# Kernel optimization log

Measured on AMD Instinct MI355X. Metric: run time of the kernel, lower is better.

## Reference

```python
import jax, jax.numpy as jnp
import numpy as np

HIDDEN = 1024
HEADS = 16
HEAD_DIM = HIDDEN // HEADS
SCALE = HEAD_DIM ** -0.5


def setup_inputs() -> dict:
    key = jax.random.key(0)
    kx, kw, ko = jax.random.split(key, 3)
    x = jax.random.normal(kx, (2, 2048, HIDDEN), dtype=jnp.float32)
    # nn.Linear(hidden, 3*hidden, bias=False): weight shape [3*hidden, hidden]
    w_qkv = jax.random.normal(kw, (3 * HIDDEN, HIDDEN), dtype=jnp.float32) * (HIDDEN ** -0.5)
    w_out = jax.random.normal(ko, (HIDDEN, HIDDEN), dtype=jnp.float32) * (HIDDEN ** -0.5)
    return {"x": x, "w_qkv": w_qkv, "w_out": w_out}


def reference(x, w_qkv, w_out):
    b, s, d = x.shape
    qkv = jnp.einsum('bsd,ed->bse', x, w_qkv)  # [b,s,3d]
    q, k, v = jnp.split(qkv, 3, axis=-1)
    def heads(t):
        return t.reshape(b, s, HEADS, HEAD_DIM).transpose(0, 2, 1, 3)  # [b,h,s,hd]
    q, k, v = heads(q), heads(k), heads(v)
    scores = jnp.einsum('bhqd,bhkd->bhqk', q, k) * SCALE
    attn = jax.nn.softmax(scores, axis=-1)
    out = jnp.einsum('bhqk,bhkd->bhqd', attn, v)
    out = out.transpose(0, 2, 1, 3).reshape(b, s, d)
    return jnp.einsum('bsd,ed->bse', out, w_out)
```

## Files before the change

### kernel.cpp

```cpp
#include <hip/hip_runtime.h>
#include <hip/hip_bf16.h>
#include <stdint.h>

typedef __bf16 bf16;
typedef __bf16 bf16x8 __attribute__((ext_vector_type(8)));
typedef float f32x4 __attribute__((ext_vector_type(4)));

#define HIDDEN 1024
#define HEADS  16
#define HD     64
#define SEQ    2048
#define BATCH  2
#define NTOK   (BATCH*SEQ)
#define E3     (3*HIDDEN)

#define QSCALE (0.125f * 1.44269504088896f)

#if __has_builtin(__builtin_amdgcn_exp2f)
#define EXP2(x) __builtin_amdgcn_exp2f(x)
#else
#define EXP2(x) __expf((x) * 0.69314718055995f)
#endif

static __device__ __forceinline__ uint32_t pkbf(float a, float b) {
  union { bf16 h[2]; uint32_t u; } x;
  x.h[0] = (bf16)a; x.h[1] = (bf16)b;
  return x.u;
}

__global__ __launch_bounds__(256) void k_convert(
    const float* __restrict__ x, const float* __restrict__ wqkv, const float* __restrict__ wout,
    bf16* __restrict__ xb, bf16* __restrict__ wqkvb, bf16* __restrict__ woutb)
{
  const int NX = NTOK*HIDDEN/4, NW = E3*HIDDEN/4;
  int i = blockIdx.x*256 + threadIdx.x;
  const float4* s; bf16* d; int o;
  if (i < NX)            { s=(const float4*)x;    d=xb;    o=i; }
  else if (i < NX+NW)    { s=(const float4*)wqkv; d=wqkvb; o=i-NX; }
  else                   { s=(const float4*)wout; d=woutb; o=i-NX-NW; }
  float4 v = s[o];
  union { bf16 b[4]; uint2 u; } p;
  p.b[0]=(bf16)v.x; p.b[1]=(bf16)v.y; p.b[2]=(bf16)v.z; p.b[3]=(bf16)v.w;
  *(uint2*)(d + (size_t)o*4) = p.u;
}

template<int EPI, int BM>
__global__ __launch_bounds__(256) void k_gemm(
    const bf16* __restrict__ A, const bf16* __restrict__ B,
    bf16* __restrict__ Oq, bf16* __restrict__ Ok, bf16* __restrict__ Ov,
    float* __restrict__ Of, int M, int N, int K, int nbn)
{
  constexpr int MI = BM/32;
  __shared__ bf16 As[BM*64];
  __shared__ bf16 Bs[128*64];
  const int t = threadIdx.x;
  const int lane = t & 63;
  const int w = t >> 6;
  const int g = lane >> 4;
  const int l15 = lane & 15;
  const int wm = (w >> 1) * (BM/2), wn = (w & 1) * 64;
  const int bm = blockIdx.x / nbn, bn = blockIdx.x % nbn;
  const int brow = bm*BM, bcol = bn*128;

  f32x4 acc[MI][4];
  #pragma unroll
  for (int mi=0;mi<MI;mi++)
    #pragma unroll
    for (int ni=0;ni<4;ni++)
      #pragma unroll
      for (int r=0;r<4;r++) acc[mi][ni][r] = 0.f;

  const int nk = K >> 6;
  for (int kt = 0; kt < nk; ++kt) {
    #pragma unroll
    for (int j=0; j<BM/32; j++) {
      int ch = w*(BM*2) + j*64 + lane;
      int row = ch>>3, part = ch&7;
      const bf16* ga = A + (size_t)(brow+row)*K + kt*64 + (part ^ (row&7))*8;
      __builtin_amdgcn_global_load_lds((const uint32_t*)ga,
          (uint32_t*)(As + (size_t)(w*(BM*2) + j*64)*8), 16, 0, 0);
    }
    #pragma unroll
    for (int j=0; j<4; j++) {
      int ch = w*256 + j*64 + lane;
      int row = ch>>3, part = ch&7;
      const bf16* gb = B + (size_t)(bcol+row)*K + kt*64 + (part ^ (row&7))*8;
      __builtin_amdgcn_global_load_lds((const uint32_t*)gb,
          (uint32_t*)(Bs + (size_t)(w*256 + j*64)*8), 16, 0, 0);
    }
    __syncthreads();
    #pragma unroll
    for (int kc=0; kc<2; kc++) {
      bf16x8 af[MI], bfr[4];
      #pragma unroll
      for (int mi=0;mi<MI;mi++) {
        int row = wm + mi*16 + l15;
        af[mi] = *(const bf16x8*)((const char*)As + row*128 + ((kc*64 + g*16) ^ ((row&7)<<4)));
      }
      #pragma unroll
      for (int ni=0;ni<4;ni++) {
        int row = wn + ni*16 + l15;
        bfr[ni] = *(const bf16x8*)((const char*)Bs + row*128 + ((kc*64 + g*16) ^ ((row&7)<<4)));
      }
      #pragma unroll
      for (int mi=0;mi<MI;mi++)
        #pragma unroll
        for (int ni=0;ni<4;ni++)
          acc[mi][ni] = __builtin_amdgcn_mfma_f32_16x16x32_bf16(af[mi], bfr[ni], acc[mi][ni], 0, 0, 0);
    }
    __syncthreads();
  }

  #pragma unroll
  for (int mi=0;mi<MI;mi++) {
    #pragma unroll
    for (int ni=0;ni<4;ni++) {
      #pragma unroll
      for (int r=0;r<4;r++) {
        float val = acc[mi][ni][r];
        int m = brow + wm + mi*16 + 4*g + r;
        int e = bcol + wn + ni*16 + l15;
        if (EPI == 0) {
          int part = e >> 10, we = e & 1023;
          int hh = we >> 6, dd = we & 63;
          int b = m >> 11, sb = m & 2047;
          size_t idx = (((size_t)b*HEADS + hh)*SEQ + sb)*HD + dd;
          if (part == 0)      Oq[idx] = (bf16)(val * QSCALE);
          else if (part == 1) Ok[idx] = (bf16)val;
          else                Ov[idx] = (bf16)val;
        } else {
          Of[(size_t)m*HIDDEN + e] = val;
        }
      }
    }
  }
}

__global__ __launch_bounds__(256, 2) void k_attn(
    const bf16* __restrict__ Qg, const bf16* __restrict__ Kg, const bf16* __restrict__ Vg,
    bf16* __restrict__ Og)
{
  __shared__ bf16 Kl[2][64*64];
  __shared__ bf16 Vt[2][64*64];
  const int t = threadIdx.x;
  const int lane = t & 63;
  const int w = t >> 6;
  const int g = lane >> 4;
  const int q = lane & 15;
  const int bh = blockIdx.x >> 4;
  const int qb = blockIdx.x & 15;
  const int q0 = qb*128 + w*32;
  const size_t bhS = (size_t)bh * SEQ * HD;

  bf16x8 qf[2][2];
  #pragma unroll
  for (int qs=0;qs<2;qs++) {
    const bf16* qrow = Qg + bhS + (size_t)(q0 + 16*qs + q)*HD + 8*g;
    qf[qs][0] = *(const bf16x8*)(qrow);
    qf[qs][1] = *(const bf16x8*)(qrow + 32);
  }

  f32x4 ot[2][4];
  #pragma unroll
  for (int qs=0;qs<2;qs++)
    #pragma unroll
    for (int df=0;df<4;df++)
      #pragma unroll
      for (int r=0;r<4;r++) ot[qs][df][r] = 0.f;
  float mrun0 = -3.0e38f, mrun1 = -3.0e38f, lrun0 = 0.f, lrun1 = 0.f;

  const int kr0 = t >> 3, kp0 = t & 7;
  const int kv0 = (t & 31)*2;
  const int dd0 = (t >> 5)*8;
  const int kvf0 = kv0 >> 4, gv = (kv0 >> 2) & 3, rv = kv0 & 3;
  const int pos0 = 32*(kvf0 >> 1) + 8*gv + 4*(kvf0 & 1) + rv;

  auto loadK = [&](int it, uint4& a, uint4& b) {
    const bf16* p0 = Kg + bhS + (size_t)(it*64 + kr0)*HD + kp0*8;
    a = *(const uint4*)p0;
    b = *(const uint4*)(p0 + 32*HD);
  };
  auto writeK = [&](int buf, uint4 a, uint4 b) {
    int sw = (kp0 ^ (kr0 & 7)) * 16;
    char* base = (char*)&Kl[buf][0];
    *(uint4*)(base + kr0*128 + sw) = a;
    *(uint4*)(base + (kr0+32)*128 + sw) = b;
  };
  auto loadV = [&](int it, uint4& a, uint4& b) {
    const bf16* vg = Vg + bhS + (size_t)(it*64 + kv0)*HD + dd0;
    a = *(const uint4*)vg;
    b = *(const uint4*)(vg + HD);
  };
  auto writeVt = [&](int buf, uint4 va, uint4 vb) {
    const uint32_t* pa = (const uint32_t*)&va;
    const uint32_t* pb = (const uint32_t*)&vb;
    char* base = (char*)&Vt[buf][0];
    #pragma unroll
    for (int jj=0;jj<8;jj++) {
      int dd = dd0 + jj;
      uint32_t pr = __builtin_amdgcn_perm(pb[jj>>1], pa[jj>>1],
                                          (jj&1) ? 0x07060302u : 0x05040100u);
      int byte = (dd*128 + pos0*2) ^ (jj<<4);
      *(uint32_t*)(base + byte) = pr;
    }
  };

  auto doQK = [&](const char* Kbase, f32x4 (&sf)[2][4]) {
    #pragma unroll
    for (int qs=0;qs<2;qs++)
      #pragma unroll
      for (int kvf=0;kvf<4;kvf++)
        #pragma unroll
        for (int r=0;r<4;r++) sf[qs][kvf][r] = 0.f;
    __builtin_amdgcn_s_setprio(1);
    #pragma unroll
    for (int kvf=0;kvf<4;kvf++) {
      int row = 16*kvf + q;
      #pragma unroll
      for (int kc=0;kc<2;kc++) {
        int byte = row*128 + ((16*g + 64*kc) ^ ((row&7)<<4));
        bf16x8 kf = *(const bf16x8*)(Kbase + byte);
        sf[0][kvf] = __builtin_amdgcn_mfma_f32_16x16x32_bf16(kf, qf[0][kc], sf[0][kvf], 0,0,0);
        sf[1][kvf] = __builtin_amdgcn_mfma_f32_16x16x32_bf16(kf, qf[1][kc], sf[1][kvf], 0,0,0);
      }
    }
    __builtin_amdgcn_s_setprio(0);
  };

  auto doSMPV = [&](const char* Vbase, f32x4 (&sf)[2][4]) {
    float pm0 = -3.0e38f, pm1 = -3.0e38f;
    #pragma unroll
    for (int kvf=0;kvf<4;kvf++)
      #pragma unroll
      for (int r=0;r<4;r++) {
        pm0 = fmaxf(pm0, sf[0][kvf][r]);
        pm1 = fmaxf(pm1, sf[1][kvf][r]);
      }
    pm0 = fmaxf(pm0, __shfl_xor(pm0, 16, 64));
    pm0 = fmaxf(pm0, __shfl_xor(pm0, 32, 64));
    pm1 = fmaxf(pm1, __shfl_xor(pm1, 16, 64));
    pm1 = fmaxf(pm1, __shfl_xor(pm1, 32, 64));

    bool need = (pm0 - mrun0 > 8.f) || (pm1 - mrun1 > 8.f);
    if (__any(need)) {
      float mn0 = fmaxf(mrun0, pm0), mn1 = fmaxf(mrun1, pm1);
      float a0 = EXP2(mrun0 - mn0), a1 = EXP2(mrun1 - mn1);
      lrun0 *= a0; lrun1 *= a1;
      #pragma unroll
      for (int df=0;df<4;df++)
        #pragma unroll
        for (int r=0;r<4;r++) { ot[0][df][r] *= a0; ot[1][df][r] *= a1; }
      mrun0 = mn0; mrun1 = mn1;
    }
    float rs0 = 0.f, rs1 = 0.f;
    #pragma unroll
    for (int kvf=0;kvf<4;kvf++)
      #pragma unroll
      for (int r=0;r<4;r++) {
        float p0 = EXP2(sf[0][kvf][r] - mrun0); sf[0][kvf][r] = p0; rs0 += p0;
        float p1 = EXP2(sf[1][kvf][r] - mrun1); sf[1][kvf][r] = p1; rs1 += p1;
      }
    rs0 += __shfl_xor(rs0, 16, 64); rs0 += __shfl_xor(rs0, 32, 64);
    rs1 += __shfl_xor(rs1, 16, 64); rs1 += __shfl_xor(rs1, 32, 64);
    lrun0 += rs0; lrun1 += rs1;

    uint32_t pk[2][4][2];
    #pragma unroll
    for (int qs=0;qs<2;qs++)
      #pragma unroll
      for (int kvf=0;kvf<4;kvf++) {
        pk[qs][kvf][0] = pkbf(sf[qs][kvf][0], sf[qs][kvf][1]);
        pk[qs][kvf][1] = pkbf(sf[qs][kvf][2], sf[qs][kvf][3]);
      }

    __builtin_amdgcn_s_setprio(1);
    #pragma unroll
    for (int kc=0;kc<2;kc++) {
      union { uint32_t u[4]; bf16x8 v; } pf0, pf1;
      pf0.u[0] = pk[0][2*kc][0]; pf0.u[1] = pk[0][2*kc][1];
      pf0.u[2] = pk[0][2*kc+1][0]; pf0.u[3] = pk[0][2*kc+1][1];
      pf1.u[0] = pk[1][2*kc][0]; pf1.u[1] = pk[1][2*kc][1];
      pf1.u[2] = pk[1][2*kc+1][0]; pf1.u[3] = pk[1][2*kc+1][1];
      #pragma unroll
      for (int df=0;df<4;df++) {
        int row = 16*df + q;
        int byte = row*128 + ((16*g + 64*kc) ^ ((row&7)<<4));
        bf16x8 vf = *(const bf16x8*)(Vbase + byte);
        ot[0][df] = __builtin_amdgcn_mfma_f32_16x16x32_bf16(vf, pf0.v, ot[0][df], 0,0,0);
        ot[1][df] = __builtin_amdgcn_mfma_f32_16x16x32_bf16(vf, pf1.v, ot[1][df], 0,0,0);
      }
    }
    __builtin_amdgcn_s_setprio(0);
  };

  const char* K0 = (const char*)&Kl[0][0];
  const char* K1 = (const char*)&Kl[1][0];
  const char* V0 = (const char*)&Vt[0][0];
  const char* V1 = (const char*)&Vt[1][0];

  uint4 ka, kb, va, vb;
  loadK(0, ka, kb); loadV(0, va, vb);
  writeK(0, ka, kb); writeVt(0, va, vb);
  __syncthreads();
  loadK(1, ka, kb); loadV(1, va, vb);

  f32x4 sfA[2][4], sfB[2][4];
  const int NT = SEQ/64;
  for (int it = 0; it < NT; it += 2) {
    doQK(K0, sfA);
    if (it > 0) doSMPV(V1, sfB);
    __syncthreads();
    writeK(1, ka, kb); writeVt(1, va, vb);
    __syncthreads();
    if (it + 2 < NT) { loadK(it+2, ka, kb); loadV(it+2, va, vb); }
    doQK(K1, sfB);
    doSMPV(V0, sfA);
    if (it + 2 < NT) {
      __syncthreads();
      writeK(0, ka, kb); writeVt(0, va, vb);
      __syncthreads();
      if (it + 3 < NT) { loadK(it+3, ka, kb); loadV(it+3, va, vb); }
    }
  }
  doSMPV(V1, sfB);

  float inv0 = 1.0f / lrun0, inv1 = 1.0f / lrun1;
  int b = bh >> 4, head = bh & 15;
  #pragma unroll
  for (int qs=0;qs<2;qs++) {
    float inv = qs ? inv1 : inv0;
    size_t orow = ((size_t)b*SEQ + q0 + 16*qs + q)*HIDDEN + head*HD;
    #pragma unroll
    for (int df=0;df<4;df++) {
      uint2 pr;
      pr.x = pkbf(ot[qs][df][0]*inv, ot[qs][df][1]*inv);
      pr.y = pkbf(ot[qs][df][2]*inv, ot[qs][df][3]*inv);
      *(uint2*)(Og + orow + 16*df + 4*g) = pr;
    }
  }
}

extern "C" void kernel_launch(void* const* d_in, const int* in_sizes, int n_in,
                              void* d_out, int out_size, void* d_ws, size_t ws_size,
                              hipStream_t stream)
{
  (void)in_sizes; (void)n_in; (void)out_size; (void)ws_size;
  const float* x    = (const float*)d_in[0];
  const float* wqkv = (const float*)d_in[1];
  const float* wout = (const float*)d_in[2];
  float* out = (float*)d_out;
  char* ws = (char*)d_ws;
  bf16* xb    = (bf16*)(ws);
  bf16* wqkvb = (bf16*)(ws + 8388608);
  bf16* woutb = (bf16*)(ws + 14680064);
  bf16* Q     = (bf16*)(ws + 16777216);
  bf16* K     = (bf16*)(ws + 25165824);
  bf16* V     = (bf16*)(ws + 33554432);
  bf16* O     = (bf16*)(ws + 41943040);

  k_convert<<<8192, 256, 0, stream>>>(x, wqkv, wout, xb, wqkvb, woutb);
  k_gemm<0,128><<<32*24, 256, 0, stream>>>(xb, wqkvb, Q, K, V, nullptr, NTOK, E3, HIDDEN, 24);
  k_attn<<<512, 256, 0, stream>>>(Q, K, V, O);
  k_gemm<1,64><<<64*8, 256, 0, stream>>>(O, woutb, nullptr, nullptr, nullptr, out, NTOK, HIDDEN, HIDDEN, 8);
}
```

Baseline: 180.3 us.

## Load K fragments straight into registers and simplify attention pipeline

```diff
diff --git a/kernel.cpp b/kernel.cpp
--- a/kernel.cpp
+++ b/kernel.cpp
@@ -140,7 +140,6 @@
     const bf16* __restrict__ Qg, const bf16* __restrict__ Kg, const bf16* __restrict__ Vg,
     bf16* __restrict__ Og)
 {
-  __shared__ bf16 Kl[2][64*64];
   __shared__ bf16 Vt[2][64*64];
   const int t = threadIdx.x;
   const int lane = t & 63;
@@ -169,22 +168,18 @@
       for (int r=0;r<4;r++) ot[qs][df][r] = 0.f;
   float mrun0 = -3.0e38f, mrun1 = -3.0e38f, lrun0 = 0.f, lrun1 = 0.f;
 
-  const int kr0 = t >> 3, kp0 = t & 7;
   const int kv0 = (t & 31)*2;
   const int dd0 = (t >> 5)*8;
   const int kvf0 = kv0 >> 4, gv = (kv0 >> 2) & 3, rv = kv0 & 3;
   const int pos0 = 32*(kvf0 >> 1) + 8*gv + 4*(kvf0 & 1) + rv;
 
-  auto loadK = [&](int it, uint4& a, uint4& b) {
-    const bf16* p0 = Kg + bhS + (size_t)(it*64 + kr0)*HD + kp0*8;
-    a = *(const uint4*)p0;
-    b = *(const uint4*)(p0 + 32*HD);
-  };
-  auto writeK = [&](int buf, uint4 a, uint4 b) {
-    int sw = (kp0 ^ (kr0 & 7)) * 16;
-    char* base = (char*)&Kl[buf][0];
-    *(uint4*)(base + kr0*128 + sw) = a;
-    *(uint4*)(base + (kr0+32)*128 + sw) = b;
+  auto loadKreg = [&](int it, bf16x8 (&kf)[4][2]) {
+    const bf16* kb = Kg + bhS + (size_t)(it*64 + q)*HD + 8*g;
+    #pragma unroll
+    for (int kvf=0;kvf<4;kvf++) {
+      kf[kvf][0] = *(const bf16x8*)(kb + (size_t)(16*kvf)*HD);
+      kf[kvf][1] = *(const bf16x8*)(kb + (size_t)(16*kvf)*HD + 32);
+    }
   };
   auto loadV = [&](int it, uint4& a, uint4& b) {
     const bf16* vg = Vg + bhS + (size_t)(it*64 + kv0)*HD + dd0;
@@ -205,7 +200,8 @@
     }
   };
 
-  auto doQK = [&](const char* Kbase, f32x4 (&sf)[2][4]) {
+  auto phase = [&](const bf16x8 (&kf)[4][2], const char* Vbase) {
+    f32x4 sf[2][4];
     #pragma unroll
     for (int qs=0;qs<2;qs++)
       #pragma unroll
@@ -214,20 +210,14 @@
         for (int r=0;r<4;r++) sf[qs][kvf][r] = 0.f;
     __builtin_amdgcn_s_setprio(1);
     #pragma unroll
-    for (int kvf=0;kvf<4;kvf++) {
-      int row = 16*kvf + q;
+    for (int kvf=0;kvf<4;kvf++)
       #pragma unroll
       for (int kc=0;kc<2;kc++) {
-        int byte = row*128 + ((16*g + 64*kc) ^ ((row&7)<<4));
-        bf16x8 kf = *(const bf16x8*)(Kbase + byte);
-        sf[0][kvf] = __builtin_amdgcn_mfma_f32_16x16x32_bf16(kf, qf[0][kc], sf[0][kvf], 0,0,0);
-        sf[1][kvf] = __builtin_amdgcn_mfma_f32_16x16x32_bf16(kf, qf[1][kc], sf[1][kvf], 0,0,0);
-      }
-    }
+        sf[0][kvf] = __builtin_amdgcn_mfma_f32_16x16x32_bf16(kf[kvf][kc], qf[0][kc], sf[0][kvf], 0,0,0);
+        sf[1][kvf] = __builtin_amdgcn_mfma_f32_16x16x32_bf16(kf[kvf][kc], qf[1][kc], sf[1][kvf], 0,0,0);
+      }
     __builtin_amdgcn_s_setprio(0);
-  };
-
-  auto doSMPV = [&](const char* Vbase, f32x4 (&sf)[2][4]) {
+
     float pm0 = -3.0e38f, pm1 = -3.0e38f;
     #pragma unroll
     for (int kvf=0;kvf<4;kvf++)
@@ -293,36 +283,31 @@
     __builtin_amdgcn_s_setprio(0);
   };
 
-  const char* K0 = (const char*)&Kl[0][0];
-  const char* K1 = (const char*)&Kl[1][0];
   const char* V0 = (const char*)&Vt[0][0];
   const char* V1 = (const char*)&Vt[1][0];
 
-  uint4 ka, kb, va, vb;
-  loadK(0, ka, kb); loadV(0, va, vb);
-  writeK(0, ka, kb); writeVt(0, va, vb);
+  bf16x8 kA[4][2], kB[4][2];
+  uint4 va, vb;
+  loadKreg(0, kA);
+  loadV(0, va, vb);
+  writeVt(0, va, vb);
   __syncthreads();
-  loadK(1, ka, kb); loadV(1, va, vb);
-
-  f32x4 sfA[2][4], sfB[2][4];
+  loadV(1, va, vb);
+  loadKreg(1, kB);
+
   const int NT = SEQ/64;
   for (int it = 0; it < NT; it += 2) {
-    doQK(K0, sfA);
-    if (it > 0) doSMPV(V1, sfB);
+    phase(kA, V0);
+    if (it+2 < NT) loadKreg(it+2, kA);
+    writeVt(1, va, vb);
+    if (it+2 < NT) loadV(it+2, va, vb);
     __syncthreads();
-    writeK(1, ka, kb); writeVt(1, va, vb);
+    phase(kB, V1);
+    if (it+3 < NT) loadKreg(it+3, kB);
+    if (it+2 < NT) writeVt(0, va, vb);
+    if (it+3 < NT) loadV(it+3, va, vb);
     __syncthreads();
-    if (it + 2 < NT) { loadK(it+2, ka, kb); loadV(it+2, va, vb); }
-    doQK(K1, sfB);
-    doSMPV(V0, sfA);
-    if (it + 2 < NT) {
-      __syncthreads();
-      writeK(0, ka, kb); writeVt(0, va, vb);
-      __syncthreads();
-      if (it + 3 < NT) { loadK(it+3, ka, kb); loadV(it+3, va, vb); }
-    }
-  }
-  doSMPV(V1, sfB);
+  }
 
   float inv0 = 1.0f / lrun0, inv1 = 1.0f / lrun1;
   int b = bh >> 4, head = bh & 15;
```

Measured after the change: 212.5 us. +17.9%, slower.
